# Optimization experiments

Measured on AMD Instinct MI355X. Metric: run time of the kernel, lower is better.

Reference implementation:

```python
import jax, jax.numpy as jnp
import numpy as np

DILATED_KS = (7, 7)   # dilated_kernel_size (Hk, Wk)
SCALING = 1.0
GROUPS = 1
STRIDE = (1, 1)
PADDING = (3, 3)


def construct_kernel(weight, P):
    """Bilinear scatter-add of kernel_count weighted points into a dense
    (out, in//g, Hk, Wk) kernel. weight: (O, Cg, K), P: (2, Cg, K)."""
    Hk, Wk = DILATED_KS
    lim_h, lim_w = Hk // 2, Wk // 2
    O, Cg, K = weight.shape
    ph = jnp.clip(P[0] * SCALING, -lim_h, lim_h) + lim_h    # (Cg, K) in [0, Hk-1]
    pw = jnp.clip(P[1] * SCALING, -lim_w, lim_w) + lim_w    # (Cg, K) in [0, Wk-1]
    ih = jnp.floor(ph).astype(jnp.int32)
    iw = jnp.floor(pw).astype(jnp.int32)
    rh = ph - ih
    rw = pw - iw
    cidx = jnp.broadcast_to(jnp.arange(Cg)[:, None], (Cg, K))
    kern = jnp.zeros((O, Cg, Hk, Wk), dtype=weight.dtype)
    corners = [(0, 0, (1 - rh) * (1 - rw)),
               (0, 1, (1 - rh) * rw),
               (1, 0, rh * (1 - rw)),
               (1, 1, rh * rw)]
    for di, dj, frac in corners:
        # out-of-range corners (at the boundary) have zero frac; 'drop' discards them
        kern = kern.at[:, cidx, ih + di, iw + dj].add(weight * frac[None], mode='drop')
    return kern


def setup_inputs() -> dict:
    key = jax.random.key(0)
    k1, k2, k3, k4 = jax.random.split(key, 4)
    x = jax.random.normal(k1, (32, 128, 56, 56), dtype=jnp.float32)
    weight = jax.random.normal(k2, (128, 128, 9), dtype=jnp.float32) * 0.05
    P = jax.random.normal(k3, (2, 128, 9), dtype=jnp.float32)  # positions ~ N(0,1), clamped in fwd
    bias = jax.random.normal(k4, (128,), dtype=jnp.float32) * 0.05
    return {"x": x, "weight": weight, "P": P, "bias": bias}


def reference(x, weight, P, bias):
    kern = construct_kernel(weight, P)  # (O, Cg, 7, 7)
    out = jax.lax.conv_general_dilated(
        x, kern,
        window_strides=STRIDE,
        padding=[(PADDING[0], PADDING[0]), (PADDING[1], PADDING[1])],
        dimension_numbers=('NCHW', 'OIHW', 'NCHW'),
        feature_group_count=GROUPS)
    return out + bias[None, :, None, None]
```

## Files before the change

### kernel.cpp

```cpp
#include <hip/hip_runtime.h>
#include <stdint.h>

typedef short v8s __attribute__((ext_vector_type(8)));
typedef float v4f __attribute__((ext_vector_type(4)));

#define KS    7
#define KPTS  9
#define OCH   128
#define CCH   128
#define NB    32
#define HW    56
#define PAD   3
#define KTOT  (KS*KS*OCH*CCH)

#define HBLK  4
#define ROWS  10
#define WP    72
#define CCK   32
#define NCC   4
#define HP    62
#define ROWB  (WP*CCK*2)
#define XS_B  (ROWS*WP*CCK*2)
#define AB_B  (4*OCH*CCK*2)
#define SMEM_B (XS_B + AB_B)

__device__ __forceinline__ unsigned short f2bf(float f) {
  unsigned int u = __builtin_bit_cast(unsigned int, f);
  u += 0x7fffu + ((u >> 16) & 1u);
  return (unsigned short)(u >> 16);
}

__device__ __forceinline__ void gl_lds16(const void* g, void* l) {
  __builtin_amdgcn_global_load_lds(
      (const __attribute__((address_space(1))) unsigned int*)g,
      (__attribute__((address_space(3))) unsigned int*)l, 16, 0, 0);
}

__global__ void scatter_kern(const float* __restrict__ wgt,
                             const float* __restrict__ P,
                             float* __restrict__ kf) {
  const int c = blockIdx.x, k = blockIdx.y, o = threadIdx.x;
  const float p0 = P[c*KPTS + k];
  const float p1 = P[CCH*KPTS + c*KPTS + k];
  const float ph = fminf(fmaxf(p0, -3.f), 3.f) + 3.f;
  const float pw = fminf(fmaxf(p1, -3.f), 3.f) + 3.f;
  const int ih = (int)floorf(ph), iw = (int)floorf(pw);
  const float rh = ph - (float)ih, rw = pw - (float)iw;
  const float wt = wgt[(o*CCH + c)*KPTS + k];
  const float f00 = (1.f-rh)*(1.f-rw);
  const float f01 = (1.f-rh)*rw;
  const float f10 = rh*(1.f-rw);
  const float f11 = rh*rw;
  atomicAdd(&kf[((ih*KS + iw)*OCH + o)*CCH + c], wt*f00);
  if (iw+1 < KS) atomicAdd(&kf[((ih*KS + iw+1)*OCH + o)*CCH + c], wt*f01);
  if (ih+1 < KS) atomicAdd(&kf[(((ih+1)*KS + iw)*OCH + o)*CCH + c], wt*f10);
  if (ih+1 < KS && iw+1 < KS) atomicAdd(&kf[(((ih+1)*KS + iw+1)*OCH + o)*CCH + c], wt*f11);
}

__global__ void cvt_kern(const float* __restrict__ kf, unsigned short* __restrict__ kb) {
  int i = blockIdx.x * 256 + threadIdx.x;
  if (i >= KTOT) return;
  const int c    = i & 127;
  const int o    = (i >> 7) & 127;
  const int khkw = i >> 14;
  const int cc = c >> 5, sc = (c >> 3) & 3, cl = c & 7;
  const int pc = sc ^ ((o >> 1) & 3);
  kb[(((size_t)(cc*49 + khkw)*OCH + o)*CCK) + pc*8 + cl] = f2bf(kf[i]);
}

__global__ __launch_bounds__(256) void xpose(const float* __restrict__ x,
                                             unsigned short* __restrict__ xt) {
  __shared__ unsigned short lb[CCK][HW + 2];
  const int hp = blockIdx.x;
  const int cc = blockIdx.y;
  const int n  = blockIdx.z;
  const int t  = threadIdx.x;
  const int h  = hp - PAD;
  const bool valid = (unsigned)h < (unsigned)HW;
  if (valid) {
    const float* xb = x + ((size_t)(n*CCH + cc*CCK)*HW + h)*HW;
    #pragma unroll
    for (int k = 0; k < 7; ++k) {
      const int j = k*256 + t;
      const int c = j / HW, w = j % HW;
      lb[c][w] = f2bf(xb[(size_t)c*HW*HW + w]);
    }
  }
  __syncthreads();
  unsigned short* orow = xt + (size_t)((n*NCC + cc)*HP + hp)*(WP*CCK);
  for (int q = t; q < WP*4; q += 256) {
    const int wq = q >> 2, pc = q & 3;
    const int s  = pc ^ ((wq >> 1) & 3);
    v8s v = (v8s){0,0,0,0,0,0,0,0};
    const int w = wq - PAD;
    if (valid && (unsigned)w < (unsigned)HW) {
      #pragma unroll
      for (int jj = 0; jj < 8; ++jj) v[jj] = (short)lb[s*8 + jj][w];
    }
    *(v8s*)&orow[wq*CCK + pc*8] = v;
  }
}

__global__ __launch_bounds__(256, 2) void dcls_conv(
    const unsigned short* __restrict__ xt, const unsigned short* __restrict__ kb,
    const float* __restrict__ bias, float* __restrict__ out)
{
  extern __shared__ char smem[];
  unsigned short* xs = (unsigned short*)smem;
  unsigned short* ab = (unsigned short*)(smem + XS_B);

  const int n   = blockIdx.x;
  const int hb  = blockIdx.y;
  const int tid = threadIdx.x;
  const int lane = tid & 63;
  const int wv   = tid >> 6;
  const int col  = lane & 15;
  const int kgrp = lane >> 4;

  v4f acc[8][4];
  #pragma unroll
  for (int m = 0; m < 8; ++m)
    #pragma unroll
    for (int t = 0; t < 4; ++t)
      acc[m][t] = (v4f){0.f,0.f,0.f,0.f};

  for (int cc = 0; cc < NCC; ++cc) {
    const char* src = (const char*)xt + (size_t)((n*NCC + cc)*HP + hb*HBLK)*ROWB;
    for (int i = wv; i < 45; i += 4)
      gl_lds16(src + i*1024 + lane*16, (char*)xs + i*1024);
    const char* ks = (const char*)kb + (size_t)cc*49*8192;
    #pragma unroll
    for (int u = 0; u < 2; ++u)
      #pragma unroll
      for (int j = 0; j < 2; ++j)
        gl_lds16(ks + u*8192 + wv*2048 + j*1024 + lane*16,
                 (char*)ab + u*8192 + wv*2048 + j*1024);
    __syncthreads();

    for (int ph = 0; ph < 25; ++ph) {
      const int t0 = 2*ph;
      #pragma unroll
      for (int u = 2; u < 4; ++u) {
        const int t = t0 + u;
        if (t < 49) {
          #pragma unroll
          for (int j = 0; j < 2; ++j)
            gl_lds16(ks + (size_t)t*8192 + wv*2048 + j*1024 + lane*16,
                     (char*)ab + (size_t)(t & 3)*8192 + wv*2048 + j*1024);
        }
      }
      #pragma unroll
      for (int u = 0; u < 2; ++u) {
        const int t = t0 + u;
        if (t < 49) {
          const int kh = t / 7, kw = t - kh*7;
          const int r = wv + kh;
          const unsigned short* abuf = ab + (size_t)(t & 3)*(OCH*CCK);
          v8s a[8];
          #pragma unroll
          for (int mt = 0; mt < 8; ++mt) {
            const int o = mt*16 + col;
            a[mt] = *(const v8s*)&abuf[o*CCK + ((kgrp ^ ((o >> 1) & 3)) << 3)];
          }
          __builtin_amdgcn_s_setprio(1);
          #pragma unroll
          for (int nt = 0; nt < 4; ++nt) {
            const int wp = nt*16 + col + kw;
            const v8s b = *(const v8s*)&xs[(r*WP + wp)*CCK + ((kgrp ^ ((wp >> 1) & 3)) << 3)];
            #pragma unroll
            for (int mt = 0; mt < 8; ++mt)
              acc[mt][nt] = __builtin_amdgcn_mfma_f32_16x16x32_bf16(a[mt], b, acc[mt][nt], 0, 0, 0);
          }
          __builtin_amdgcn_s_setprio(0);
        }
      }
      __syncthreads();
    }
  }

  const int h = hb*HBLK + wv;
  #pragma unroll
  for (int mt = 0; mt < 8; ++mt) {
    #pragma unroll
    for (int rr = 0; rr < 4; ++rr) {
      const int o = mt*16 + (lane >> 4)*4 + rr;
      const float bs = bias[o];
      #pragma unroll
      for (int nt = 0; nt < 4; ++nt) {
        const int w = nt*16 + col;
        if (w < HW)
          out[((size_t)(n*OCH + o)*HW + h)*HW + w] = acc[mt][nt][rr] + bs;
      }
    }
  }
}

extern "C" void kernel_launch(void* const* d_in, const int* in_sizes, int n_in,
                              void* d_out, int out_size, void* d_ws, size_t ws_size,
                              hipStream_t stream) {
  const float* x    = (const float*)d_in[0];
  const float* wgt  = (const float*)d_in[1];
  const float* P    = (const float*)d_in[2];
  const float* bias = (const float*)d_in[3];
  float* out = (float*)d_out;

  float*          kf = (float*)d_ws;
  unsigned short* kb = (unsigned short*)((char*)d_ws + (size_t)KTOT*4);
  unsigned short* xt = (unsigned short*)((char*)d_ws + (size_t)KTOT*6);

  hipFuncSetAttribute((const void*)dcls_conv,
                      hipFuncAttributeMaxDynamicSharedMemorySize, SMEM_B);

  hipMemsetAsync(kf, 0, (size_t)KTOT*4, stream);
  scatter_kern<<<dim3(CCH, KPTS), OCH, 0, stream>>>(wgt, P, kf);
  cvt_kern<<<KTOT/256, 256, 0, stream>>>(kf, kb);
  xpose<<<dim3(HP, NCC, NB), 256, 0, stream>>>(x, xt);
  dcls_conv<<<dim3(NB, HW/HBLK), 256, SMEM_B, stream>>>(xt, kb, bias, out);
}
```

Before: 197.6 us.

## Fuse kernel construction into one LDS kernel and software-pipeline conv fragment loads

```diff
diff --git a/kernel.cpp b/kernel.cpp
--- a/kernel.cpp
+++ b/kernel.cpp
@@ -11,7 +11,6 @@
 #define NB    32
 #define HW    56
 #define PAD   3
-#define KTOT  (KS*KS*OCH*CCH)
 
 #define HBLK  4
 #define ROWS  10
@@ -23,6 +22,7 @@
 #define XS_B  (ROWS*WP*CCK*2)
 #define AB_B  (4*OCH*CCK*2)
 #define SMEM_B (XS_B + AB_B)
+#define KB_BYTES ((size_t)NCC*49*OCH*CCK*2)
 
 __device__ __forceinline__ unsigned short f2bf(float f) {
   unsigned int u = __builtin_bit_cast(unsigned int, f);
@@ -36,36 +36,29 @@
       (__attribute__((address_space(3))) unsigned int*)l, 16, 0, 0);
 }
 
-__global__ void scatter_kern(const float* __restrict__ wgt,
-                             const float* __restrict__ P,
-                             float* __restrict__ kf) {
-  const int c = blockIdx.x, k = blockIdx.y, o = threadIdx.x;
-  const float p0 = P[c*KPTS + k];
-  const float p1 = P[CCH*KPTS + c*KPTS + k];
-  const float ph = fminf(fmaxf(p0, -3.f), 3.f) + 3.f;
-  const float pw = fminf(fmaxf(p1, -3.f), 3.f) + 3.f;
-  const int ih = (int)floorf(ph), iw = (int)floorf(pw);
-  const float rh = ph - (float)ih, rw = pw - (float)iw;
-  const float wt = wgt[(o*CCH + c)*KPTS + k];
-  const float f00 = (1.f-rh)*(1.f-rw);
-  const float f01 = (1.f-rh)*rw;
-  const float f10 = rh*(1.f-rw);
-  const float f11 = rh*rw;
-  atomicAdd(&kf[((ih*KS + iw)*OCH + o)*CCH + c], wt*f00);
-  if (iw+1 < KS) atomicAdd(&kf[((ih*KS + iw+1)*OCH + o)*CCH + c], wt*f01);
-  if (ih+1 < KS) atomicAdd(&kf[(((ih+1)*KS + iw)*OCH + o)*CCH + c], wt*f10);
-  if (ih+1 < KS && iw+1 < KS) atomicAdd(&kf[(((ih+1)*KS + iw+1)*OCH + o)*CCH + c], wt*f11);
-}
-
-__global__ void cvt_kern(const float* __restrict__ kf, unsigned short* __restrict__ kb) {
-  int i = blockIdx.x * 256 + threadIdx.x;
-  if (i >= KTOT) return;
-  const int c    = i & 127;
-  const int o    = (i >> 7) & 127;
-  const int khkw = i >> 14;
+__global__ __launch_bounds__(128) void build_kern(
+    const float* __restrict__ wgt, const float* __restrict__ P,
+    unsigned short* __restrict__ kb) {
+  __shared__ float sm[OCH*49];
+  const int c = blockIdx.x, o = threadIdx.x;
+  float* mine = &sm[o*49];
+  #pragma unroll
+  for (int j = 0; j < 49; ++j) mine[j] = 0.f;
+  for (int k = 0; k < KPTS; ++k) {
+    const float ph = fminf(fmaxf(P[c*KPTS + k], -3.f), 3.f) + 3.f;
+    const float pw = fminf(fmaxf(P[CCH*KPTS + c*KPTS + k], -3.f), 3.f) + 3.f;
+    const int ih = (int)floorf(ph), iw = (int)floorf(pw);
+    const float rh = ph - (float)ih, rw = pw - (float)iw;
+    const float wt = wgt[(o*CCH + c)*KPTS + k];
+    mine[ih*KS + iw] += wt*(1.f-rh)*(1.f-rw);
+    if (iw+1 < KS) mine[ih*KS + iw+1] += wt*(1.f-rh)*rw;
+    if (ih+1 < KS) mine[(ih+1)*KS + iw] += wt*rh*(1.f-rw);
+    if (ih+1 < KS && iw+1 < KS) mine[(ih+1)*KS + iw+1] += wt*rh*rw;
+  }
   const int cc = c >> 5, sc = (c >> 3) & 3, cl = c & 7;
   const int pc = sc ^ ((o >> 1) & 3);
-  kb[(((size_t)(cc*49 + khkw)*OCH + o)*CCK) + pc*8 + cl] = f2bf(kf[i]);
+  for (int tap = 0; tap < 49; ++tap)
+    kb[(((size_t)(cc*49 + tap)*OCH + o)*CCK) + pc*8 + cl] = f2bf(mine[tap]);
 }
 
 __global__ __launch_bounds__(256) void xpose(const float* __restrict__ x,
@@ -101,6 +94,17 @@
   }
 }
 
+#define MFMA_TAP(FA, FB)                                                      \
+  __builtin_amdgcn_s_setprio(1);                                              \
+  _Pragma("unroll")                                                           \
+  for (int nt = 0; nt < 4; ++nt) {                                            \
+    _Pragma("unroll")                                                         \
+    for (int mt = 0; mt < 8; ++mt)                                            \
+      acc[mt][nt] = __builtin_amdgcn_mfma_f32_16x16x32_bf16(FA[mt], FB[nt],   \
+                                                            acc[mt][nt], 0, 0, 0); \
+  }                                                                           \
+  __builtin_amdgcn_s_setprio(0);
+
 __global__ __launch_bounds__(256, 2) void dcls_conv(
     const unsigned short* __restrict__ xt, const unsigned short* __restrict__ kb,
     const float* __restrict__ bias, float* __restrict__ out)
@@ -116,6 +120,7 @@
   const int wv   = tid >> 6;
   const int col  = lane & 15;
   const int kgrp = lane >> 4;
+  const int swA  = (kgrp ^ ((col >> 1) & 3)) << 3;
 
   v4f acc[8][4];
   #pragma unroll
@@ -123,6 +128,8 @@
     #pragma unroll
     for (int t = 0; t < 4; ++t)
       acc[m][t] = (v4f){0.f,0.f,0.f,0.f};
+
+  v8s fa0[8], fa1[8], fb0[4], fb1[4];
 
   for (int cc = 0; cc < NCC; ++cc) {
     const char* src = (const char*)xt + (size_t)((n*NCC + cc)*HP + hb*HBLK)*ROWB;
@@ -137,45 +144,65 @@
                  (char*)ab + u*8192 + wv*2048 + j*1024);
     __syncthreads();
 
-    for (int ph = 0; ph < 25; ++ph) {
-      const int t0 = 2*ph;
-      #pragma unroll
-      for (int u = 2; u < 4; ++u) {
-        const int t = t0 + u;
-        if (t < 49) {
+    #pragma unroll
+    for (int mt = 0; mt < 8; ++mt)
+      fa0[mt] = *(const v8s*)&ab[(mt*16 + col)*CCK + swA];
+    {
+      const int swB = (kgrp ^ ((col >> 1) & 3)) << 3;
+      const int base = (wv*WP + col)*CCK + swB;
+      #pragma unroll
+      for (int nt = 0; nt < 4; ++nt)
+        fb0[nt] = *(const v8s*)&xs[base + nt*512];
+    }
+
+    for (int phx = 0; phx < 24; ++phx) {
+      const int t0 = 2*phx;
+      {
+        const int tp = t0 + 2;
+        #pragma unroll
+        for (int j = 0; j < 2; ++j)
+          gl_lds16(ks + (size_t)tp*8192 + wv*2048 + j*1024 + lane*16,
+                   (char*)ab + (size_t)(tp & 3)*8192 + wv*2048 + j*1024);
+        const int tq = t0 + 3;
+        if (tq < 49) {
           #pragma unroll
           for (int j = 0; j < 2; ++j)
-            gl_lds16(ks + (size_t)t*8192 + wv*2048 + j*1024 + lane*16,
-                     (char*)ab + (size_t)(t & 3)*8192 + wv*2048 + j*1024);
+            gl_lds16(ks + (size_t)tq*8192 + wv*2048 + j*1024 + lane*16,
+                     (char*)ab + (size_t)(tq & 3)*8192 + wv*2048 + j*1024);
         }
       }
-      #pragma unroll
-      for (int u = 0; u < 2; ++u) {
-        const int t = t0 + u;
-        if (t < 49) {
-          const int kh = t / 7, kw = t - kh*7;
-          const int r = wv + kh;
-          const unsigned short* abuf = ab + (size_t)(t & 3)*(OCH*CCK);
-          v8s a[8];
-          #pragma unroll
-          for (int mt = 0; mt < 8; ++mt) {
-            const int o = mt*16 + col;
-            a[mt] = *(const v8s*)&abuf[o*CCK + ((kgrp ^ ((o >> 1) & 3)) << 3)];
-          }
-          __builtin_amdgcn_s_setprio(1);
-          #pragma unroll
-          for (int nt = 0; nt < 4; ++nt) {
-            const int wp = nt*16 + col + kw;
-            const v8s b = *(const v8s*)&xs[(r*WP + wp)*CCK + ((kgrp ^ ((wp >> 1) & 3)) << 3)];
-            #pragma unroll
-            for (int mt = 0; mt < 8; ++mt)
-              acc[mt][nt] = __builtin_amdgcn_mfma_f32_16x16x32_bf16(a[mt], b, acc[mt][nt], 0, 0, 0);
-          }
-          __builtin_amdgcn_s_setprio(0);
-        }
-      }
+      {
+        const int t = t0 + 1, kh = t/7, kw = t - kh*7, r = wv + kh;
+        const unsigned short* ap = ab + (size_t)(t & 3)*(OCH*CCK);
+        #pragma unroll
+        for (int mt = 0; mt < 8; ++mt)
+          fa1[mt] = *(const v8s*)&ap[(mt*16 + col)*CCK + swA];
+        const int swB = (kgrp ^ (((col + kw) >> 1) & 3)) << 3;
+        const int base = (r*WP + col + kw)*CCK + swB;
+        #pragma unroll
+        for (int nt = 0; nt < 4; ++nt)
+          fb1[nt] = *(const v8s*)&xs[base + nt*512];
+      }
+      MFMA_TAP(fa0, fb0)
+      {
+        const int t = t0 + 2, kh = t/7, kw = t - kh*7, r = wv + kh;
+        const int swB = (kgrp ^ (((col + kw) >> 1) & 3)) << 3;
+        const int base = (r*WP + col + kw)*CCK + swB;
+        #pragma unroll
+        for (int nt = 0; nt < 4; ++nt)
+          fb0[nt] = *(const v8s*)&xs[base + nt*512];
+      }
+      MFMA_TAP(fa1, fb1)
       __syncthreads();
-    }
+      {
+        const unsigned short* ap = ab + (size_t)((t0 + 2) & 3)*(OCH*CCK);
+        #pragma unroll
+        for (int mt = 0; mt < 8; ++mt)
+          fa0[mt] = *(const v8s*)&ap[(mt*16 + col)*CCK + swA];
+      }
+    }
+    MFMA_TAP(fa0, fb0)
+    __syncthreads();
   }
 
   const int h = hb*HBLK + wv;
@@ -204,16 +231,13 @@
   const float* bias = (const float*)d_in[3];
   float* out = (float*)d_out;
 
-  float*          kf = (float*)d_ws;
-  unsigned short* kb = (unsigned short*)((char*)d_ws + (size_t)KTOT*4);
-  unsigned short* xt = (unsigned short*)((char*)d_ws + (size_t)KTOT*6);
+  unsigned short* kb = (unsigned short*)d_ws;
+  unsigned short* xt = (unsigned short*)((char*)d_ws + (2u<<20));
 
   hipFuncSetAttribute((const void*)dcls_conv,
                       hipFuncAttributeMaxDynamicSharedMemorySize, SMEM_B);
 
-  hipMemsetAsync(kf, 0, (size_t)KTOT*4, stream);
-  scatter_kern<<<dim3(CCH, KPTS), OCH, 0, stream>>>(wgt, P, kf);
-  cvt_kern<<<KTOT/256, 256, 0, stream>>>(kf, kb);
+  build_kern<<<CCH, OCH, 0, stream>>>(wgt, P, kb);
   xpose<<<dim3(HP, NCC, NB), 256, 0, stream>>>(x, xt);
   dcls_conv<<<dim3(NB, HW/HBLK), 256, SMEM_B, stream>>>(xt, kb, bias, out);
 }
```

Measured after the change: 159.3 us. 19.4% less time.
